# Kernel tuning notes

Hardware: AMD Instinct MI355X
Metric: run time of the kernel (lower is better)

Reference implementation:

```python
import jax, jax.numpy as jnp
import numpy as np

N_NODES = 100000
N_EDGES = 1600000
D = 128


def _graph_conv(x, src, dst, norm_src, norm_dst, W, b):
    # DGL GraphConv, norm='both': out = D_dst^{-1/2} A D_src^{-1/2} x W + b
    xs = x * norm_src[:, None]                 # [N, d] scale by src (out-)degree
    agg = jax.ops.segment_sum(xs[src], dst, num_segments=N_NODES)  # SpMM
    hd = agg * norm_dst[:, None]
    return hd @ W + b


def setup_inputs() -> dict:
    key = jax.random.key(0)
    ks = jax.random.split(key, 9)
    h = jax.random.normal(ks[0], (N_NODES, D), dtype=jnp.float32)
    src = jax.random.randint(ks[1], (N_EDGES,), 0, N_NODES, dtype=jnp.int64)
    dst = jax.random.randint(ks[2], (N_EDGES,), 0, N_NODES, dtype=jnp.int64)
    s = 1.0 / np.sqrt(D)
    W0 = jax.random.uniform(ks[3], (D, D), jnp.float32, -s, s)
    b0 = jnp.zeros((D,), jnp.float32)
    W1 = jax.random.uniform(ks[4], (D, D), jnp.float32, -s, s)
    b1 = jnp.zeros((D,), jnp.float32)
    W2 = jax.random.uniform(ks[5], (D, D), jnp.float32, -s, s)
    b2 = jnp.zeros((D,), jnp.float32)
    return {"h": h, "src": src, "dst": dst, "W0": W0, "b0": b0,
            "W1": W1, "b1": b1, "W2": W2, "b2": b2}


def reference(h, src, dst, W0, b0, W1, b1, W2, b2):
    ones = jnp.ones((N_EDGES,), jnp.float32)
    deg_out = jnp.maximum(jax.ops.segment_sum(ones, src, num_segments=N_NODES), 1.0)
    deg_in = jnp.maximum(jax.ops.segment_sum(ones, dst, num_segments=N_NODES), 1.0)
    norm_src = deg_out ** -0.5
    norm_dst = deg_in ** -0.5

    x = jax.nn.relu(_graph_conv(h, src, dst, norm_src, norm_dst, W0, b0))
    x = jax.nn.relu(_graph_conv(x, src, dst, norm_src, norm_dst, W1, b1))
    x = _graph_conv(x, src, dst, norm_src, norm_dst, W2, b2)
    # dgl.mean_nodes over a single graph -> [1, out_size]
    return jnp.mean(x, axis=0, keepdims=True)
```

## Files before the change

### kernel.cpp

```cpp
#include <hip/hip_runtime.h>
#include <hip/hip_fp16.h>

#define N_NODES 100000
#define N_EDGES 1600000
#define D 128
#define SCAN_NB ((N_NODES + 1023) / 1024)
#define CHK 128
#define CHUNK_E (N_EDGES / CHK)
#define HALF_N 50000
#define HALF_U (HALF_N / 4)
#define PP_STRIDE (N_NODES / 4)
#define NSH4 4
#define SH4 (N_NODES / NSH4)
#define SH4_U (SH4 / 4)

typedef _Float16 f16x4 __attribute__((ext_vector_type(4)));
typedef _Float16 f16x8 __attribute__((ext_vector_type(8)));
typedef float f32x4 __attribute__((ext_vector_type(4)));
typedef float f32x2 __attribute__((ext_vector_type(2)));

__global__ __launch_bounds__(256) void
k_hist(const int* __restrict__ src, const int* __restrict__ dst,
       unsigned int* __restrict__ pp) {
    __shared__ unsigned int h[HALF_U];
    int b = blockIdx.x;
    int arr = b >> 8, half = (b >> 7) & 1, c = b & (CHK - 1);
    const int* a = arr ? dst : src;
    int lo = half * HALF_N;
    for (int i = threadIdx.x; i < HALF_U; i += 256) h[i] = 0;
    __syncthreads();
    int e0 = c * CHUNK_E;
    for (int i = e0 + threadIdx.x; i < e0 + CHUNK_E; i += 256) {
        int v = a[i] - lo;
        if ((unsigned)v < HALF_N)
            atomicAdd(&h[v >> 2], 1u << ((v & 3) * 8));
    }
    __syncthreads();
    unsigned int* po = pp + ((size_t)(arr * CHK + c)) * PP_STRIDE + half * HALF_U;
    for (int i = threadIdx.x; i < HALF_U; i += 256) po[i] = h[i];
}

__global__ void k_merge(unsigned int* __restrict__ pp,
                        int* __restrict__ cnt_src, int* __restrict__ cnt_dst) {
    int g = blockIdx.x * blockDim.x + threadIdx.x;
    if (g >= 2 * PP_STRIDE) return;
    int arr = g / PP_STRIDE, u = g % PP_STRIDE;
    unsigned int* p = pp + ((size_t)arr * CHK) * PP_STRIDE + u;
    int s0 = 0, s1 = 0, s2 = 0, s3 = 0;
#pragma unroll 8
    for (int c = 0; c < CHK; c++) {
        unsigned int v = p[(size_t)c * PP_STRIDE];
        p[(size_t)c * PP_STRIDE] =
            (unsigned)s0 | ((unsigned)s1 << 8) | ((unsigned)s2 << 16) | ((unsigned)s3 << 24);
        s0 += v & 255; s1 += (v >> 8) & 255; s2 += (v >> 16) & 255; s3 += (v >> 24) & 255;
    }
    int* cnt = arr ? cnt_dst : cnt_src;
    cnt[4 * u + 0] = s0; cnt[4 * u + 1] = s1; cnt[4 * u + 2] = s2; cnt[4 * u + 3] = s3;
}

__global__ __launch_bounds__(1024) void
k_scan1(const int* __restrict__ cnt_dst, const int* __restrict__ cnt_src,
        int* __restrict__ rpD, int* __restrict__ rpS,
        int* __restrict__ bsD, int* __restrict__ bsS) {
    __shared__ int s[1024];
    int arr = blockIdx.x / SCAN_NB, bb = blockIdx.x % SCAN_NB;
    const int* cnt = arr ? cnt_src : cnt_dst;
    int* rp1 = (arr ? rpS : rpD) + 1;
    int* bs = arr ? bsS : bsD;
    int tid = threadIdx.x;
    int i = bb * 1024 + tid;
    int v = (i < N_NODES) ? cnt[i] : 0;
    s[tid] = v;
    __syncthreads();
    for (int d = 1; d < 1024; d <<= 1) {
        int t = (tid >= d) ? s[tid - d] : 0;
        __syncthreads();
        s[tid] += t;
        __syncthreads();
    }
    if (i < N_NODES) rp1[i] = s[tid];
    if (tid == 1023) bs[bb] = s[1023];
}

__global__ void k_scan2(int* __restrict__ bsD, int* __restrict__ bsS) {
    __shared__ int s[128];
    int* bs = blockIdx.x ? bsS : bsD;
    int tid = threadIdx.x;
    int v = (tid < SCAN_NB) ? bs[tid] : 0;
    s[tid] = v;
    __syncthreads();
    for (int d = 1; d < 128; d <<= 1) {
        int t = (tid >= d) ? s[tid - d] : 0;
        __syncthreads();
        s[tid] += t;
        __syncthreads();
    }
    if (tid < SCAN_NB) bs[tid] = s[tid] - v;
}

__global__ void k_scan3norm(int* __restrict__ rpD, int* __restrict__ rpS,
                            const int* __restrict__ bsD, const int* __restrict__ bsS,
                            const int* __restrict__ cnt_src, const int* __restrict__ cnt_dst,
                            float* __restrict__ ns, float* __restrict__ nd) {
    int i = blockIdx.x * blockDim.x + threadIdx.x;
    if (i >= N_NODES) return;
    rpD[1 + i] += bsD[i >> 10];
    rpS[1 + i] += bsS[i >> 10];
    if (i == 0) { rpD[0] = 0; rpS[0] = 0; }
    ns[i] = rsqrtf((float)max(cnt_src[i], 1));
    nd[i] = rsqrtf((float)max(cnt_dst[i], 1));
}

__global__ __launch_bounds__(256) void
k_scatter_dst(const int* __restrict__ src, const int* __restrict__ dst,
              const int* __restrict__ rpD, const unsigned int* __restrict__ pp,
              int* __restrict__ csr_src) {
    __shared__ unsigned int cur[SH4_U];
    int sh = blockIdx.x & 3, c = blockIdx.x >> 2;
    int lo = sh * SH4;
    const unsigned int* pre = pp + ((size_t)(CHK + c)) * PP_STRIDE;
    for (int i = threadIdx.x; i < SH4_U; i += 256) cur[i] = 0;
    __syncthreads();
    int e0 = c * CHUNK_E;
    for (int i = e0 + threadIdx.x; i < e0 + CHUNK_E; i += 256) {
        int dfull = dst[i];
        int d = dfull - lo;
        if ((unsigned)d < SH4) {
            int sft = (d & 3) * 8;
            int rank = (atomicAdd(&cur[d >> 2], 1u << sft) >> sft) & 255;
            int p8 = (pre[dfull >> 2] >> ((dfull & 3) * 8)) & 255;
            csr_src[rpD[dfull] + p8 + rank] = src[i];
        }
    }
}

__global__ __launch_bounds__(256) void
k_scatter_src(const int* __restrict__ src, const int* __restrict__ dst,
              const int* __restrict__ rpS, const unsigned int* __restrict__ pp,
              const float* __restrict__ nd, float* __restrict__ csrv) {
    __shared__ unsigned int cur[SH4_U];
    int sh = blockIdx.x & 3, c = blockIdx.x >> 2;
    int lo = sh * SH4;
    const unsigned int* pre = pp + (size_t)c * PP_STRIDE;
    for (int i = threadIdx.x; i < SH4_U; i += 256) cur[i] = 0;
    __syncthreads();
    int e0 = c * CHUNK_E;
    for (int i = e0 + threadIdx.x; i < e0 + CHUNK_E; i += 256) {
        int sfull = src[i];
        int s = sfull - lo;
        if ((unsigned)s < SH4) {
            int sft = (s & 3) * 8;
            int rank = (atomicAdd(&cur[s >> 2], 1u << sft) >> sft) & 255;
            int p8 = (pre[sfull >> 2] >> ((sfull & 3) * 8)) & 255;
            csrv[rpS[sfull] + p8 + rank] = nd[dst[i]];
        }
    }
}

__global__ void k_wsum(const int* __restrict__ rpS, const float* __restrict__ csrv,
                       const float* __restrict__ ns, float* __restrict__ wsum) {
    int gid = blockIdx.x * blockDim.x + threadIdx.x;
    int wv = gid >> 6, lane = gid & 63;
    int n = wv * 16 + (lane & 15);
    int off = lane >> 4;
    float s = 0.0f;
    int beg = 0, end = 0;
    if (n < N_NODES) { beg = rpS[n]; end = rpS[n + 1]; }
    for (int j = beg + off; j < end; j += 4) s += csrv[j];
    s += __shfl_xor(s, 16, 64);
    s += __shfl_xor(s, 32, 64);
    if (n < N_NODES && lane < 16) wsum[n] = s * ns[n];
}

__global__ void k_prep_w(const float* __restrict__ W0, const float* __restrict__ W1,
                         __half* __restrict__ Wt) {
    int i = blockIdx.x * blockDim.x + threadIdx.x;
    if (i >= 2 * D * D) return;
    int l = i >> 14, r = i & (D * D - 1);
    int n = r >> 7, k = r & 127;
    const float* W = l ? W1 : W0;
    Wt[i] = __float2half(W[k * D + n]);
}

__global__ void k_scale_rows(const float* __restrict__ x, const float* __restrict__ ns,
                             unsigned int* __restrict__ out) {
    int i = blockIdx.x * blockDim.x + threadIdx.x;
    if (i >= N_NODES * (D / 4)) return;
    int n = i >> 5;
    float4 v = ((const float4*)x)[i];
    float s = ns[n];
    int u = __builtin_amdgcn_cvt_pk_fp8_f32(v.x * s, v.y * s, 0, false);
    u = __builtin_amdgcn_cvt_pk_fp8_f32(v.z * s, v.w * s, u, true);
    out[i] = (unsigned int)u;
}

__global__ __launch_bounds__(256) void
k_spmm(const unsigned char* __restrict__ x8, const int* __restrict__ row_ptr,
       const int* __restrict__ csr_src, __half* __restrict__ agg) {
    int wave = (blockIdx.x * blockDim.x + threadIdx.x) >> 6;
    int lane = threadIdx.x & 63;
    int hf = lane >> 5, l32 = lane & 31;
    if (wave >= N_NODES) return;
    int beg = row_ptr[wave], end = row_ptr[wave + 1];
    float a0 = 0.f, a1 = 0.f, a2 = 0.f, a3 = 0.f;
    int j = beg;
    for (; j + 7 < end; j += 8) {
#pragma unroll
        for (int p = 0; p < 4; p++) {
            int s0 = csr_src[j + 2 * p];
            int s1 = csr_src[j + 2 * p + 1];
            int s = hf ? s1 : s0;
            unsigned int u = *(const unsigned int*)(x8 + (size_t)s * D + 4 * l32);
            f32x2 lo = __builtin_amdgcn_cvt_pk_f32_fp8(u, false);
            f32x2 hi = __builtin_amdgcn_cvt_pk_f32_fp8(u, true);
            a0 += lo[0]; a1 += lo[1]; a2 += hi[0]; a3 += hi[1];
        }
    }
    for (; j + 1 < end; j += 2) {
        int s0 = csr_src[j], s1 = csr_src[j + 1];
        int s = hf ? s1 : s0;
        unsigned int u = *(const unsigned int*)(x8 + (size_t)s * D + 4 * l32);
        f32x2 lo = __builtin_amdgcn_cvt_pk_f32_fp8(u, false);
        f32x2 hi = __builtin_amdgcn_cvt_pk_f32_fp8(u, true);
        a0 += lo[0]; a1 += lo[1]; a2 += hi[0]; a3 += hi[1];
    }
    if (j < end && hf == 0) {
        int s = csr_src[j];
        unsigned int u = *(const unsigned int*)(x8 + (size_t)s * D + 4 * l32);
        f32x2 lo = __builtin_amdgcn_cvt_pk_f32_fp8(u, false);
        f32x2 hi = __builtin_amdgcn_cvt_pk_f32_fp8(u, true);
        a0 += lo[0]; a1 += lo[1]; a2 += hi[0]; a3 += hi[1];
    }
    a0 += __shfl_xor(a0, 32, 64);
    a1 += __shfl_xor(a1, 32, 64);
    a2 += __shfl_xor(a2, 32, 64);
    a3 += __shfl_xor(a3, 32, 64);
    if (hf == 0) {
        f16x4 o;
        o[0] = (_Float16)a0; o[1] = (_Float16)a1; o[2] = (_Float16)a2; o[3] = (_Float16)a3;
        ((f16x4*)(agg + (size_t)wave * D))[l32] = o;
    }
}

__global__ __launch_bounds__(256) void
k_gemm_mfma(const __half* __restrict__ A, const __half* __restrict__ Wt,
            const float* __restrict__ b, const float* __restrict__ nd,
            const float* __restrict__ ns, unsigned char* __restrict__ out) {
    int w = threadIdx.x >> 6, lane = threadIdx.x & 63;
    int m = lane & 15, q = lane >> 4;
    int row0 = blockIdx.x * 128 + w * 32;

    f16x8 zf;
#pragma unroll
    for (int j = 0; j < 8; j++) zf[j] = (_Float16)0;
    f16x8 af[2][4];
#pragma unroll
    for (int g = 0; g < 2; g++) {
        int arow = row0 + g * 16 + m;
        const f16x8* pa = (const f16x8*)(A + (size_t)arow * D);
        bool aok = arow < N_NODES;
#pragma unroll
        for (int ks = 0; ks < 4; ks++) af[g][ks] = aok ? pa[ks * 4 + q] : zf;
    }

    const f16x8* pb = (const f16x8*)Wt;
    f32x4 acc[2][8];
#pragma unroll
    for (int g = 0; g < 2; g++)
#pragma unroll
        for (int nt = 0; nt < 8; nt++) acc[g][nt] = (f32x4){0.f, 0.f, 0.f, 0.f};

#pragma unroll
    for (int ks = 0; ks < 4; ks++) {
#pragma unroll
        for (int nt = 0; nt < 8; nt++) {
            f16x8 bf = pb[((nt * 16 + m) << 4) + (ks << 2) + q];
            acc[0][nt] = __builtin_amdgcn_mfma_f32_16x16x32_f16(af[0][ks], bf, acc[0][nt], 0, 0, 0);
            acc[1][nt] = __builtin_amdgcn_mfma_f32_16x16x32_f16(af[1][ks], bf, acc[1][nt], 0, 0, 0);
        }
    }

#pragma unroll
    for (int g = 0; g < 2; g++) {
        int er = row0 + g * 16 + q * 4;
        float sd[4], ss[4];
#pragma unroll
        for (int r = 0; r < 4; r++) {
            int n = er + r;
            bool ok = n < N_NODES;
            sd[r] = ok ? nd[n] : 0.0f;
            ss[r] = ok ? ns[n] : 0.0f;
        }
#pragma unroll
        for (int nt = 0; nt < 8; nt++) {
            int col = nt * 16 + m;
            float bc = b[col];
#pragma unroll
            for (int r = 0; r < 4; r++) {
                int n = er + r;
                if (n < N_NODES) {
                    float v = fmaxf(sd[r] * acc[g][nt][r] + bc, 0.0f) * ss[r];
                    int pk = __builtin_amdgcn_cvt_pk_fp8_f32(v, v, 0, false);
                    out[(size_t)n * D + col] = (unsigned char)(pk & 0xff);
                }
            }
        }
    }
}

__global__ __launch_bounds__(256) void
k_gemm_red(const __half* __restrict__ A, const __half* __restrict__ Wt,
           const float* __restrict__ b, const float* __restrict__ nd,
           const float* __restrict__ wsum, float* __restrict__ colsum) {
    __shared__ float red[128];
    int tid = threadIdx.x;
    if (tid < 128) red[tid] = 0.0f;
    __syncthreads();

    int w = tid >> 6, lane = tid & 63;
    int m = lane & 15, q = lane >> 4;
    int row0 = blockIdx.x * 128 + w * 32;

    f16x8 zf;
#pragma unroll
    for (int j = 0; j < 8; j++) zf[j] = (_Float16)0;
    f16x8 af[2][4];
#pragma unroll
    for (int g = 0; g < 2; g++) {
        int arow = row0 + g * 16 + m;
        const f16x8* pa = (const f16x8*)(A + (size_t)arow * D);
        bool aok = arow < N_NODES;
#pragma unroll
        for (int ks = 0; ks < 4; ks++) af[g][ks] = aok ? pa[ks * 4 + q] : zf;
    }

    const f16x8* pb = (const f16x8*)Wt;
    f32x4 acc[2][8];
#pragma unroll
    for (int g = 0; g < 2; g++)
#pragma unroll
        for (int nt = 0; nt < 8; nt++) acc[g][nt] = (f32x4){0.f, 0.f, 0.f, 0.f};

#pragma unroll
    for (int ks = 0; ks < 4; ks++) {
#pragma unroll
        for (int nt = 0; nt < 8; nt++) {
            f16x8 bf = pb[((nt * 16 + m) << 4) + (ks << 2) + q];
            acc[0][nt] = __builtin_amdgcn_mfma_f32_16x16x32_f16(af[0][ks], bf, acc[0][nt], 0, 0, 0);
            acc[1][nt] = __builtin_amdgcn_mfma_f32_16x16x32_f16(af[1][ks], bf, acc[1][nt], 0, 0, 0);
        }
    }

    float sd[2][4], sw[2][4];
#pragma unroll
    for (int g = 0; g < 2; g++) {
        int er = row0 + g * 16 + q * 4;
#pragma unroll
        for (int r = 0; r < 4; r++) {
            int n = er + r;
            bool ok = n < N_NODES;
            sd[g][r] = ok ? nd[n] : 0.0f;
            sw[g][r] = ok ? wsum[n] : 0.0f;
        }
    }
#pragma unroll
    for (int nt = 0; nt < 8; nt++) {
        int col = nt * 16 + m;
        float bc = b[col];
        float pc = 0.0f;
#pragma unroll
        for (int g = 0; g < 2; g++)
#pragma unroll
            for (int r = 0; r < 4; r++)
                pc += sw[g][r] * fmaxf(sd[g][r] * acc[g][nt][r] + bc, 0.0f);
        atomicAdd(&red[col], pc);
    }
    __syncthreads();
    if (tid < 128) unsafeAtomicAdd(&colsum[tid], red[tid]);
}

__global__ void k_final(const float* __restrict__ colsum, const float* __restrict__ W,
                        const float* __restrict__ b, float* __restrict__ out) {
    __shared__ float m[128];
    int j = threadIdx.x;
    m[j] = colsum[j] * (1.0f / N_NODES);
    __syncthreads();
    float acc = b[j];
    for (int k = 0; k < 128; k++)
        acc = fmaf(m[k], W[(size_t)k * D + j], acc);
    out[j] = acc;
}

extern "C" void kernel_launch(void* const* d_in, const int* in_sizes, int n_in,
                              void* d_out, int out_size, void* d_ws, size_t ws_size,
                              hipStream_t stream) {
    const float* h   = (const float*)d_in[0];
    const int*   src = (const int*)d_in[1];
    const int*   dst = (const int*)d_in[2];
    const float* W0  = (const float*)d_in[3];
    const float* b0  = (const float*)d_in[4];
    const float* W1  = (const float*)d_in[5];
    const float* b1  = (const float*)d_in[6];
    const float* W2  = (const float*)d_in[7];
    const float* b2  = (const float*)d_in[8];
    float* out = (float*)d_out;

    float*         ns      = (float*)d_ws;
    float*         nd      = ns + N_NODES;
    float*         wsum    = nd + N_NODES;
    float*         colsum  = wsum + N_NODES;
    int*           rpD     = (int*)(colsum + 128);
    int*           rpS     = rpD + N_NODES + 1;
    int*           cnt_src = rpS + N_NODES + 1;
    int*           cnt_dst = cnt_src + N_NODES;
    int*           bsD     = cnt_dst + N_NODES;
    int*           bsS     = bsD + 128;
    __half*        Wt16    = (__half*)(bsS + 128);
    int*           csr_src = (int*)(Wt16 + 2 * D * D);
    float*         csrv    = (float*)(csr_src + N_EDGES);
    unsigned int*  pp      = (unsigned int*)(csrv + N_EDGES);
    unsigned char* x8      = (unsigned char*)pp;
    __half*        agg16   = (__half*)(pp + 2 * (size_t)CHK * PP_STRIDE);

    k_hist<<<2 * 2 * CHK, 256, 0, stream>>>(src, dst, pp);
    k_merge<<<(2 * PP_STRIDE + 255) / 256, 256, 0, stream>>>(pp, cnt_src, cnt_dst);
    k_scan1<<<2 * SCAN_NB, 1024, 0, stream>>>(cnt_dst, cnt_src, rpD, rpS, bsD, bsS);
    k_scan2<<<2, 128, 0, stream>>>(bsD, bsS);
    k_scan3norm<<<(N_NODES + 255) / 256, 256, 0, stream>>>(rpD, rpS, bsD, bsS,
                                                           cnt_src, cnt_dst, ns, nd);
    k_scatter_dst<<<NSH4 * CHK, 256, 0, stream>>>(src, dst, rpD, pp, csr_src);
    k_scatter_src<<<NSH4 * CHK, 256, 0, stream>>>(src, dst, rpS, pp, nd, csrv);
    k_wsum<<<(N_NODES * 4 + 255) / 256, 256, 0, stream>>>(rpS, csrv, ns, wsum);

    k_prep_w<<<(2 * D * D + 255) / 256, 256, 0, stream>>>(W0, W1, Wt16);
    k_scale_rows<<<(N_NODES * (D / 4) + 255) / 256, 256, 0, stream>>>(h, ns, (unsigned int*)x8);
    hipMemsetAsync(colsum, 0, 128 * sizeof(float), stream);

    k_spmm<<<(N_NODES + 3) / 4, 256, 0, stream>>>(x8, rpD, csr_src, agg16);
    k_gemm_mfma<<<(N_NODES + 127) / 128, 256, 0, stream>>>(agg16, Wt16, b0, nd, ns, x8);
    k_spmm<<<(N_NODES + 3) / 4, 256, 0, stream>>>(x8, rpD, csr_src, agg16);
    k_gemm_red<<<(N_NODES + 127) / 128, 256, 0, stream>>>(agg16, Wt16 + (size_t)D * D,
                                                          b1, nd, wsum, colsum);
    k_final<<<1, 128, 0, stream>>>(colsum, W2, b2, out);
}
```

Baseline: 439.0 us.

## Fuse SpMM gather with MFMA GEMM per 128-row tile via shared memory

Each layer's SpMM aggregation now writes the aggregated fp16 rows into a padded shared-memory tile, and the MFMA GEMM and epilogue run in the same kernel. This drops the global fp16 agg round trip and two launches. Several smaller changes come with it: the weight and row-scaling prep kernels are merged, the colsum memset moves into the scan kernel, scatter shards drop from 4 to 2, and layer output ping-pongs between two fp8 buffers. The risk is lower occupancy: there are only 782 blocks of 4 waves, each wave gathers 32 rows serially, and the kernel uses about 34KB of LDS per block, which limits latency hiding for the irregular gathers.

```diff
diff --git a/kernel.cpp b/kernel.cpp
--- a/kernel.cpp
+++ b/kernel.cpp
@@ -10,9 +10,10 @@
 #define HALF_N 50000
 #define HALF_U (HALF_N / 4)
 #define PP_STRIDE (N_NODES / 4)
-#define NSH4 4
-#define SH4 (N_NODES / NSH4)
-#define SH4_U (SH4 / 4)
+#define NSH2 2
+#define SH2 (N_NODES / NSH2)
+#define SH2_U (SH2 / 4)
+#define PADH 136
 
 typedef _Float16 f16x4 __attribute__((ext_vector_type(4)));
 typedef _Float16 f16x8 __attribute__((ext_vector_type(8)));
@@ -101,12 +102,14 @@
 __global__ void k_scan3norm(int* __restrict__ rpD, int* __restrict__ rpS,
                             const int* __restrict__ bsD, const int* __restrict__ bsS,
                             const int* __restrict__ cnt_src, const int* __restrict__ cnt_dst,
-                            float* __restrict__ ns, float* __restrict__ nd) {
+                            float* __restrict__ ns, float* __restrict__ nd,
+                            float* __restrict__ colsum) {
     int i = blockIdx.x * blockDim.x + threadIdx.x;
     if (i >= N_NODES) return;
     rpD[1 + i] += bsD[i >> 10];
     rpS[1 + i] += bsS[i >> 10];
     if (i == 0) { rpD[0] = 0; rpS[0] = 0; }
+    if (i < 128) colsum[i] = 0.0f;
     ns[i] = rsqrtf((float)max(cnt_src[i], 1));
     nd[i] = rsqrtf((float)max(cnt_dst[i], 1));
 }
@@ -115,17 +118,17 @@
 k_scatter_dst(const int* __restrict__ src, const int* __restrict__ dst,
               const int* __restrict__ rpD, const unsigned int* __restrict__ pp,
               int* __restrict__ csr_src) {
-    __shared__ unsigned int cur[SH4_U];
-    int sh = blockIdx.x & 3, c = blockIdx.x >> 2;
-    int lo = sh * SH4;
+    __shared__ unsigned int cur[SH2_U];
+    int sh = blockIdx.x & 1, c = blockIdx.x >> 1;
+    int lo = sh * SH2;
     const unsigned int* pre = pp + ((size_t)(CHK + c)) * PP_STRIDE;
-    for (int i = threadIdx.x; i < SH4_U; i += 256) cur[i] = 0;
+    for (int i = threadIdx.x; i < SH2_U; i += 256) cur[i] = 0;
     __syncthreads();
     int e0 = c * CHUNK_E;
     for (int i = e0 + threadIdx.x; i < e0 + CHUNK_E; i += 256) {
         int dfull = dst[i];
         int d = dfull - lo;
-        if ((unsigned)d < SH4) {
+        if ((unsigned)d < SH2) {
             int sft = (d & 3) * 8;
             int rank = (atomicAdd(&cur[d >> 2], 1u << sft) >> sft) & 255;
             int p8 = (pre[dfull >> 2] >> ((dfull & 3) * 8)) & 255;
@@ -138,17 +141,17 @@
 k_scatter_src(const int* __restrict__ src, const int* __restrict__ dst,
               const int* __restrict__ rpS, const unsigned int* __restrict__ pp,
               const float* __restrict__ nd, float* __restrict__ csrv) {
-    __shared__ unsigned int cur[SH4_U];
-    int sh = blockIdx.x & 3, c = blockIdx.x >> 2;
-    int lo = sh * SH4;
+    __shared__ unsigned int cur[SH2_U];
+    int sh = blockIdx.x & 1, c = blockIdx.x >> 1;
+    int lo = sh * SH2;
     const unsigned int* pre = pp + (size_t)c * PP_STRIDE;
-    for (int i = threadIdx.x; i < SH4_U; i += 256) cur[i] = 0;
+    for (int i = threadIdx.x; i < SH2_U; i += 256) cur[i] = 0;
     __syncthreads();
     int e0 = c * CHUNK_E;
     for (int i = e0 + threadIdx.x; i < e0 + CHUNK_E; i += 256) {
         int sfull = src[i];
         int s = sfull - lo;
-        if ((unsigned)s < SH4) {
+        if ((unsigned)s < SH2) {
             int sft = (s & 3) * 8;
             int rank = (atomicAdd(&cur[s >> 2], 1u << sft) >> sft) & 255;
             int p8 = (pre[sfull >> 2] >> ((sfull & 3) * 8)) & 255;
@@ -172,19 +175,18 @@
     if (n < N_NODES && lane < 16) wsum[n] = s * ns[n];
 }
 
-__global__ void k_prep_w(const float* __restrict__ W0, const float* __restrict__ W1,
-                         __half* __restrict__ Wt) {
-    int i = blockIdx.x * blockDim.x + threadIdx.x;
-    if (i >= 2 * D * D) return;
-    int l = i >> 14, r = i & (D * D - 1);
-    int n = r >> 7, k = r & 127;
-    const float* W = l ? W1 : W0;
-    Wt[i] = __float2half(W[k * D + n]);
-}
-
-__global__ void k_scale_rows(const float* __restrict__ x, const float* __restrict__ ns,
-                             unsigned int* __restrict__ out) {
-    int i = blockIdx.x * blockDim.x + threadIdx.x;
+__global__ void k_prep(const float* __restrict__ W0, const float* __restrict__ W1,
+                       __half* __restrict__ Wt, const float* __restrict__ x,
+                       const float* __restrict__ ns, unsigned int* __restrict__ out) {
+    if (blockIdx.x < 128) {
+        int i = blockIdx.x * 256 + threadIdx.x;
+        int l = i >> 14, r = i & (D * D - 1);
+        int n = r >> 7, k = r & 127;
+        const float* W = l ? W1 : W0;
+        Wt[i] = __float2half(W[k * D + n]);
+        return;
+    }
+    int i = (blockIdx.x - 128) * 256 + threadIdx.x;
     if (i >= N_NODES * (D / 4)) return;
     int n = i >> 5;
     float4 v = ((const float4*)x)[i];
@@ -194,75 +196,66 @@
     out[i] = (unsigned int)u;
 }
 
-__global__ __launch_bounds__(256) void
-k_spmm(const unsigned char* __restrict__ x8, const int* __restrict__ row_ptr,
-       const int* __restrict__ csr_src, __half* __restrict__ agg) {
-    int wave = (blockIdx.x * blockDim.x + threadIdx.x) >> 6;
-    int lane = threadIdx.x & 63;
+template <int MODE>
+__device__ void fused_layer(const unsigned char* __restrict__ x8,
+                            const int* __restrict__ rpD, const int* __restrict__ csr_src,
+                            const __half* __restrict__ Wt, const float* __restrict__ b,
+                            const float* __restrict__ nd, const float* __restrict__ ns_or_w,
+                            unsigned char* __restrict__ out8, float* __restrict__ colsum,
+                            _Float16* As, float* red) {
+    int tid = threadIdx.x;
+    int w = tid >> 6, lane = tid & 63;
     int hf = lane >> 5, l32 = lane & 31;
-    if (wave >= N_NODES) return;
-    int beg = row_ptr[wave], end = row_ptr[wave + 1];
-    float a0 = 0.f, a1 = 0.f, a2 = 0.f, a3 = 0.f;
-    int j = beg;
-    for (; j + 7 < end; j += 8) {
-#pragma unroll
-        for (int p = 0; p < 4; p++) {
-            int s0 = csr_src[j + 2 * p];
-            int s1 = csr_src[j + 2 * p + 1];
-            int s = hf ? s1 : s0;
-            unsigned int u = *(const unsigned int*)(x8 + (size_t)s * D + 4 * l32);
-            f32x2 lo = __builtin_amdgcn_cvt_pk_f32_fp8(u, false);
-            f32x2 hi = __builtin_amdgcn_cvt_pk_f32_fp8(u, true);
-            a0 += lo[0]; a1 += lo[1]; a2 += hi[0]; a3 += hi[1];
-        }
-    }
-    for (; j + 1 < end; j += 2) {
-        int s0 = csr_src[j], s1 = csr_src[j + 1];
-        int s = hf ? s1 : s0;
-        unsigned int u = *(const unsigned int*)(x8 + (size_t)s * D + 4 * l32);
-        f32x2 lo = __builtin_amdgcn_cvt_pk_f32_fp8(u, false);
-        f32x2 hi = __builtin_amdgcn_cvt_pk_f32_fp8(u, true);
-        a0 += lo[0]; a1 += lo[1]; a2 += hi[0]; a3 += hi[1];
-    }
-    if (j < end && hf == 0) {
-        int s = csr_src[j];
-        unsigned int u = *(const unsigned int*)(x8 + (size_t)s * D + 4 * l32);
-        f32x2 lo = __builtin_amdgcn_cvt_pk_f32_fp8(u, false);
-        f32x2 hi = __builtin_amdgcn_cvt_pk_f32_fp8(u, true);
-        a0 += lo[0]; a1 += lo[1]; a2 += hi[0]; a3 += hi[1];
-    }
-    a0 += __shfl_xor(a0, 32, 64);
-    a1 += __shfl_xor(a1, 32, 64);
-    a2 += __shfl_xor(a2, 32, 64);
-    a3 += __shfl_xor(a3, 32, 64);
-    if (hf == 0) {
-        f16x4 o;
-        o[0] = (_Float16)a0; o[1] = (_Float16)a1; o[2] = (_Float16)a2; o[3] = (_Float16)a3;
-        ((f16x4*)(agg + (size_t)wave * D))[l32] = o;
-    }
-}
-
-__global__ __launch_bounds__(256) void
-k_gemm_mfma(const __half* __restrict__ A, const __half* __restrict__ Wt,
-            const float* __restrict__ b, const float* __restrict__ nd,
-            const float* __restrict__ ns, unsigned char* __restrict__ out) {
-    int w = threadIdx.x >> 6, lane = threadIdx.x & 63;
+    int row0 = blockIdx.x * 128;
+    if (MODE == 1 && tid < 128) red[tid] = 0.0f;
+
+    for (int rr = 0; rr < 32; rr++) {
+        int node = row0 + w * 32 + rr;
+        float a0 = 0.f, a1 = 0.f, a2 = 0.f, a3 = 0.f;
+        if (node < N_NODES) {
+            int beg = rpD[node], end = rpD[node + 1];
+            int j = beg;
+            for (; j + 7 < end; j += 8) {
+#pragma unroll
+                for (int p = 0; p < 4; p++) {
+                    int s0 = csr_src[j + 2 * p];
+                    int s1 = csr_src[j + 2 * p + 1];
+                    int s = hf ? s1 : s0;
+                    unsigned int u = *(const unsigned int*)(x8 + (size_t)s * D + 4 * l32);
+                    f32x2 lo = __builtin_amdgcn_cvt_pk_f32_fp8(u, false);
+                    f32x2 hi = __builtin_amdgcn_cvt_pk_f32_fp8(u, true);
+                    a0 += lo[0]; a1 += lo[1]; a2 += hi[0]; a3 += hi[1];
+                }
+            }
+            for (; j + 1 < end; j += 2) {
+                int s0 = csr_src[j], s1 = csr_src[j + 1];
+                int s = hf ? s1 : s0;
+                unsigned int u = *(const unsigned int*)(x8 + (size_t)s * D + 4 * l32);
+                f32x2 lo = __builtin_amdgcn_cvt_pk_f32_fp8(u, false);
+                f32x2 hi = __builtin_amdgcn_cvt_pk_f32_fp8(u, true);
+                a0 += lo[0]; a1 += lo[1]; a2 += hi[0]; a3 += hi[1];
+            }
+            if (j < end && hf == 0) {
+                int s = csr_src[j];
+                unsigned int u = *(const unsigned int*)(x8 + (size_t)s * D + 4 * l32);
+                f32x2 lo = __builtin_amdgcn_cvt_pk_f32_fp8(u, false);
+                f32x2 hi = __builtin_amdgcn_cvt_pk_f32_fp8(u, true);
+                a0 += lo[0]; a1 += lo[1]; a2 += hi[0]; a3 += hi[1];
+            }
+        }
+        a0 += __shfl_xor(a0, 32, 64);
+        a1 += __shfl_xor(a1, 32, 64);
+        a2 += __shfl_xor(a2, 32, 64);
+        a3 += __shfl_xor(a3, 32, 64);
+        if (hf == 0) {
+            f16x4 o;
+            o[0] = (_Float16)a0; o[1] = (_Float16)a1; o[2] = (_Float16)a2; o[3] = (_Float16)a3;
+            *(f16x4*)(As + (size_t)(w * 32 + rr) * PADH + l32 * 4) = o;
+        }
+    }
+    __syncthreads();
+
     int m = lane & 15, q = lane >> 4;
-    int row0 = blockIdx.x * 128 + w * 32;
-
-    f16x8 zf;
-#pragma unroll
-    for (int j = 0; j < 8; j++) zf[j] = (_Float16)0;
-    f16x8 af[2][4];
-#pragma unroll
-    for (int g = 0; g < 2; g++) {
-        int arow = row0 + g * 16 + m;
-        const f16x8* pa = (const f16x8*)(A + (size_t)arow * D);
-        bool aok = arow < N_NODES;
-#pragma unroll
-        for (int ks = 0; ks < 4; ks++) af[g][ks] = aok ? pa[ks * 4 + q] : zf;
-    }
-
     const f16x8* pb = (const f16x8*)Wt;
     f32x4 acc[2][8];
 #pragma unroll
@@ -272,111 +265,90 @@
 
 #pragma unroll
     for (int ks = 0; ks < 4; ks++) {
+        f16x8 a0f = *(const f16x8*)(As + (size_t)(w * 32 + m) * PADH + ks * 32 + q * 8);
+        f16x8 a1f = *(const f16x8*)(As + (size_t)(w * 32 + 16 + m) * PADH + ks * 32 + q * 8);
 #pragma unroll
         for (int nt = 0; nt < 8; nt++) {
             f16x8 bf = pb[((nt * 16 + m) << 4) + (ks << 2) + q];
-            acc[0][nt] = __builtin_amdgcn_mfma_f32_16x16x32_f16(af[0][ks], bf, acc[0][nt], 0, 0, 0);
-            acc[1][nt] = __builtin_amdgcn_mfma_f32_16x16x32_f16(af[1][ks], bf, acc[1][nt], 0, 0, 0);
-        }
-    }
-
-#pragma unroll
-    for (int g = 0; g < 2; g++) {
-        int er = row0 + g * 16 + q * 4;
-        float sd[4], ss[4];
-#pragma unroll
-        for (int r = 0; r < 4; r++) {
-            int n = er + r;
-            bool ok = n < N_NODES;
-            sd[r] = ok ? nd[n] : 0.0f;
-            ss[r] = ok ? ns[n] : 0.0f;
+            acc[0][nt] = __builtin_amdgcn_mfma_f32_16x16x32_f16(a0f, bf, acc[0][nt], 0, 0, 0);
+            acc[1][nt] = __builtin_amdgcn_mfma_f32_16x16x32_f16(a1f, bf, acc[1][nt], 0, 0, 0);
+        }
+    }
+
+    if (MODE == 0) {
+#pragma unroll
+        for (int g = 0; g < 2; g++) {
+            int er = row0 + w * 32 + g * 16 + q * 4;
+            float sd[4], ss[4];
+#pragma unroll
+            for (int r = 0; r < 4; r++) {
+                int n = er + r;
+                bool ok = n < N_NODES;
+                sd[r] = ok ? nd[n] : 0.0f;
+                ss[r] = ok ? ns_or_w[n] : 0.0f;
+            }
+#pragma unroll
+            for (int nt = 0; nt < 8; nt++) {
+                int col = nt * 16 + m;
+                float bc = b[col];
+#pragma unroll
+                for (int r = 0; r < 4; r++) {
+                    int n = er + r;
+                    if (n < N_NODES) {
+                        float v = fmaxf(sd[r] * acc[g][nt][r] + bc, 0.0f) * ss[r];
+                        int pk = __builtin_amdgcn_cvt_pk_fp8_f32(v, v, 0, false);
+                        out8[(size_t)n * D + col] = (unsigned char)(pk & 0xff);
+                    }
+                }
+            }
+        }
+    } else {
+        float sd[2][4], sw[2][4];
+#pragma unroll
+        for (int g = 0; g < 2; g++) {
+            int er = row0 + w * 32 + g * 16 + q * 4;
+#pragma unroll
+            for (int r = 0; r < 4; r++) {
+                int n = er + r;
+                bool ok = n < N_NODES;
+                sd[g][r] = ok ? nd[n] : 0.0f;
+                sw[g][r] = ok ? ns_or_w[n] : 0.0f;
+            }
         }
 #pragma unroll
         for (int nt = 0; nt < 8; nt++) {
             int col = nt * 16 + m;
             float bc = b[col];
-#pragma unroll
-            for (int r = 0; r < 4; r++) {
-                int n = er + r;
-                if (n < N_NODES) {
-                    float v = fmaxf(sd[r] * acc[g][nt][r] + bc, 0.0f) * ss[r];
-                    int pk = __builtin_amdgcn_cvt_pk_fp8_f32(v, v, 0, false);
-                    out[(size_t)n * D + col] = (unsigned char)(pk & 0xff);
-                }
-            }
-        }
+            float pc = 0.0f;
+#pragma unroll
+            for (int g = 0; g < 2; g++)
+#pragma unroll
+                for (int r = 0; r < 4; r++)
+                    pc += sw[g][r] * fmaxf(sd[g][r] * acc[g][nt][r] + bc, 0.0f);
+            atomicAdd(&red[col], pc);
+        }
+        __syncthreads();
+        if (tid < 128) unsafeAtomicAdd(&colsum[tid], red[tid]);
     }
 }
 
 __global__ __launch_bounds__(256) void
-k_gemm_red(const __half* __restrict__ A, const __half* __restrict__ Wt,
+k_fused_l0(const unsigned char* __restrict__ x8, const int* __restrict__ rpD,
+           const int* __restrict__ csr_src, const __half* __restrict__ Wt,
            const float* __restrict__ b, const float* __restrict__ nd,
-           const float* __restrict__ wsum, float* __restrict__ colsum) {
+           const float* __restrict__ ns, unsigned char* __restrict__ out8) {
+    __shared__ _Float16 As[128 * PADH];
+    fused_layer<0>(x8, rpD, csr_src, Wt, b, nd, ns, out8, nullptr, As, nullptr);
+}
+
+__global__ __launch_bounds__(256) void
+k_fused_red(const unsigned char* __restrict__ x8, const int* __restrict__ rpD,
+            const int* __restrict__ csr_src, const __half* __restrict__ Wt,
+            const float* __restrict__ b, const float* __restrict__ nd,
+            const float* __restrict__ wsum, float* __restrict__ colsum) {
+    __shared__ _Float16 As[128 * PADH];
     __shared__ float red[128];
-    int tid = threadIdx.x;
-    if (tid < 128) red[tid] = 0.0f;
-    __syncthreads();
-
-    int w = tid >> 6, lane = tid & 63;
-    int m = lane & 15, q = lane >> 4;
-    int row0 = blockIdx.x * 128 + w * 32;
-
-    f16x8 zf;
-#pragma unroll
-    for (int j = 0; j < 8; j++) zf[j] = (_Float16)0;
-    f16x8 af[2][4];
-#pragma unroll
-    for (int g = 0; g < 2; g++) {
-        int arow = row0 + g * 16 + m;
-        const f16x8* pa = (const f16x8*)(A + (size_t)arow * D);
-        bool aok = arow < N_NODES;
-#pragma unroll
-        for (int ks = 0; ks < 4; ks++) af[g][ks] = aok ? pa[ks * 4 + q] : zf;
-    }
-
-    const f16x8* pb = (const f16x8*)Wt;
-    f32x4 acc[2][8];
-#pragma unroll
-    for (int g = 0; g < 2; g++)
-#pragma unroll
-        for (int nt = 0; nt < 8; nt++) acc[g][nt] = (f32x4){0.f, 0.f, 0.f, 0.f};
-
-#pragma unroll
-    for (int ks = 0; ks < 4; ks++) {
-#pragma unroll
-        for (int nt = 0; nt < 8; nt++) {
-            f16x8 bf = pb[((nt * 16 + m) << 4) + (ks << 2) + q];
-            acc[0][nt] = __builtin_amdgcn_mfma_f32_16x16x32_f16(af[0][ks], bf, acc[0][nt], 0, 0, 0);
-            acc[1][nt] = __builtin_amdgcn_mfma_f32_16x16x32_f16(af[1][ks], bf, acc[1][nt], 0, 0, 0);
-        }
-    }
-
-    float sd[2][4], sw[2][4];
-#pragma unroll
-    for (int g = 0; g < 2; g++) {
-        int er = row0 + g * 16 + q * 4;
-#pragma unroll
-        for (int r = 0; r < 4; r++) {
-            int n = er + r;
-            bool ok = n < N_NODES;
-            sd[g][r] = ok ? nd[n] : 0.0f;
-            sw[g][r] = ok ? wsum[n] : 0.0f;
-        }
-    }
-#pragma unroll
-    for (int nt = 0; nt < 8; nt++) {
-        int col = nt * 16 + m;
-        float bc = b[col];
-        float pc = 0.0f;
-#pragma unroll
-        for (int g = 0; g < 2; g++)
-#pragma unroll
-            for (int r = 0; r < 4; r++)
-                pc += sw[g][r] * fmaxf(sd[g][r] * acc[g][nt][r] + bc, 0.0f);
-        atomicAdd(&red[col], pc);
-    }
-    __syncthreads();
-    if (tid < 128) unsafeAtomicAdd(&colsum[tid], red[tid]);
+    fused_layer<1>(x8, rpD, csr_src, Wt, b, nd, wsum, nullptr, colsum, As, red);
 }
 
 __global__ void k_final(const float* __restrict__ colsum, const float* __restrict__ W,
@@ -419,27 +391,26 @@
     int*           csr_src = (int*)(Wt16 + 2 * D * D);
     float*         csrv    = (float*)(csr_src + N_EDGES);
     unsigned int*  pp      = (unsigned int*)(csrv + N_EDGES);
-    unsigned char* x8      = (unsigned char*)pp;
-    __half*        agg16   = (__half*)(pp + 2 * (size_t)CHK * PP_STRIDE);
+    unsigned char* x8a     = (unsigned char*)pp;
+    unsigned char* x8b     = x8a + (size_t)N_NODES * D;
 
     k_hist<<<2 * 2 * CHK, 256, 0, stream>>>(src, dst, pp);
     k_merge<<<(2 * PP_STRIDE + 255) / 256, 256, 0, stream>>>(pp, cnt_src, cnt_dst);
     k_scan1<<<2 * SCAN_NB, 1024, 0, stream>>>(cnt_dst, cnt_src, rpD, rpS, bsD, bsS);
     k_scan2<<<2, 128, 0, stream>>>(bsD, bsS);
     k_scan3norm<<<(N_NODES + 255) / 256, 256, 0, stream>>>(rpD, rpS, bsD, bsS,
-                                                           cnt_src, cnt_dst, ns, nd);
-    k_scatter_dst<<<NSH4 * CHK, 256, 0, stream>>>(src, dst, rpD, pp, csr_src);
-    k_scatter_src<<<NSH4 * CHK, 256, 0, stream>>>(src, dst, rpS, pp, nd, csrv);
+                                                           cnt_src, cnt_dst, ns, nd, colsum);
+    k_scatter_dst<<<NSH2 * CHK, 256, 0, stream>>>(src, dst, rpD, pp, csr_src);
+    k_scatter_src<<<NSH2 * CHK, 256, 0, stream>>>(src, dst, rpS, pp, nd, csrv);
     k_wsum<<<(N_NODES * 4 + 255) / 256, 256, 0, stream>>>(rpS, csrv, ns, wsum);
 
-    k_prep_w<<<(2 * D * D + 255) / 256, 256, 0, stream>>>(W0, W1, Wt16);
-    k_scale_rows<<<(N_NODES * (D / 4) + 255) / 256, 256, 0, stream>>>(h, ns, (unsigned int*)x8);
-    hipMemsetAsync(colsum, 0, 128 * sizeof(float), stream);
-
-    k_spmm<<<(N_NODES + 3) / 4, 256, 0, stream>>>(x8, rpD, csr_src, agg16);
-    k_gemm_mfma<<<(N_NODES + 127) / 128, 256, 0, stream>>>(agg16, Wt16, b0, nd, ns, x8);
-    k_spmm<<<(N_NODES + 3) / 4, 256, 0, stream>>>(x8, rpD, csr_src, agg16);
-    k_gemm_red<<<(N_NODES + 127) / 128, 256, 0, stream>>>(agg16, Wt16 + (size_t)D * D,
-                                                          b1, nd, wsum, colsum);
+    k_prep<<<128 + (N_NODES * (D / 4) + 255) / 256, 256, 0, stream>>>(
+        W0, W1, Wt16, h, ns, (unsigned int*)x8a);
+
+    k_fused_l0<<<(N_NODES + 127) / 128, 256, 0, stream>>>(x8a, rpD, csr_src, Wt16,
+                                                          b0, nd, ns, x8b);
+    k_fused_red<<<(N_NODES + 127) / 128, 256, 0, stream>>>(x8b, rpD, csr_src,
+                                                           Wt16 + (size_t)D * D,
+                                                           b1, nd, wsum, colsum);
     k_final<<<1, 128, 0, stream>>>(colsum, W2, b2, out);
 }
```

Result: slower. 550.6 us (+25.4%).
